# Performance work log

Measured on AMD Instinct MI355X. Metric: run time of the kernel, lower is better.

The kernel has to match this reference:

```python
import jax, jax.numpy as jnp
import numpy as np

HIDDEN = 1024
D_INNER = 2048
DT_RANK = 64
STATE = 16
KCONV = 4


def setup_inputs() -> dict:
    key = jax.random.key(0)
    ks = jax.random.split(key, 9)
    s = lambda k, shape, sc=0.02: jax.random.normal(k, shape, dtype=jnp.float32) * sc
    return {
        "x": jax.random.normal(ks[0], (2, 1024, HIDDEN), dtype=jnp.float32),
        "in_proj_w": s(ks[1], (2 * D_INNER, HIDDEN)),
        "conv_w": s(ks[2], (D_INNER, 1, KCONV), 0.2),
        "conv_b": s(ks[3], (D_INNER,), 0.1),
        "x_proj_w": s(ks[4], (DT_RANK + 2 * STATE, D_INNER)),
        "dt_proj_w": s(ks[5], (D_INNER, DT_RANK), 0.1),
        "dt_proj_b": s(ks[6], (D_INNER,), 0.1),
        "A_log": s(ks[7], (D_INNER, STATE), 0.5),
        "out_proj_w": s(ks[8], (HIDDEN, D_INNER)),
    }


def _selective_scan(u, delta, A, B, C):
    # u, delta: (b,l,d); A: (d,n); B, C: (b,l,n)
    deltaA = jnp.exp(delta[..., None] * A)               # (b,l,d,n)
    dBu = (delta * u)[..., None] * B[:, :, None, :]      # (b,l,d,n)
    # scan over time axis; carry h: (b,d,n)
    deltaA_t = jnp.moveaxis(deltaA, 1, 0)                # (l,b,d,n)
    dBu_t = jnp.moveaxis(dBu, 1, 0)                      # (l,b,d,n)
    C_t = jnp.moveaxis(C, 1, 0)                          # (l,b,n)

    def step(h, inp):
        dA_i, dBu_i, C_i = inp
        h = dA_i * h + dBu_i
        y = jnp.einsum('bdn,bn->bd', h, C_i)
        return h, y

    h0 = jnp.zeros(u.shape[:1] + u.shape[2:] + (A.shape[1],), dtype=u.dtype)
    _, ys = jax.lax.scan(step, h0, (deltaA_t, dBu_t, C_t))
    return jnp.moveaxis(ys, 0, 1)                        # (b,l,d)


def reference(x, in_proj_w, conv_w, conv_b, x_proj_w, dt_proj_w, dt_proj_b, A_log, out_proj_w):
    b, l, _ = x.shape
    xr = x @ in_proj_w.T                                 # (b,l,2*d_inner)
    xs, res = jnp.split(xr, 2, axis=-1)
    # causal depthwise conv1d: pad left k-1 (matches padding=k-1 then [:l])
    xc = jnp.moveaxis(xs, 1, 2)                          # (b,d,l)
    xc = jax.lax.conv_general_dilated(
        xc, conv_w, window_strides=(1,), padding=[(KCONV - 1, 0)],
        feature_group_count=D_INNER,
        dimension_numbers=('NCH', 'OIH', 'NCH'))
    xc = xc + conv_b[None, :, None]
    xs = jnp.moveaxis(xc, 2, 1)                          # (b,l,d)
    xs = jax.nn.silu(xs)
    x_dbl = xs @ x_proj_w.T                              # (b,l,dt_rank+2n)
    dt, B, C = jnp.split(x_dbl, [DT_RANK, DT_RANK + STATE], axis=-1)
    delta = jax.nn.softplus(dt @ dt_proj_w.T + dt_proj_b)
    A = -jnp.exp(A_log.astype(jnp.float32))
    y = _selective_scan(xs, delta, A, B, C)
    y = y * jax.nn.silu(res)
    return y @ out_proj_w.T
```

## Files before the change

### kernel.cpp

```cpp
#include <hip/hip_runtime.h>

typedef unsigned short u16;
typedef __bf16 bf16x8 __attribute__((ext_vector_type(8)));
typedef float f32x4 __attribute__((ext_vector_type(4)));

__device__ inline float bf2f(u16 u) {
    unsigned int x = ((unsigned int)u) << 16;
    return __builtin_bit_cast(float, x);
}
__device__ inline u16 f2bf(float f) {
    unsigned int x = __builtin_bit_cast(unsigned int, f);
    return (u16)((x + 0x7FFFu + ((x >> 16) & 1u)) >> 16);
}
__device__ inline float sigm(float v) { return 1.f / (1.f + __expf(-v)); }
__device__ inline float ex2(float x) {
    float r; asm("v_exp_f32 %0, %1" : "=v"(r) : "v"(x)); return r;
}

__device__ __forceinline__ void gload16(const void* g, void* l) {
    __builtin_amdgcn_global_load_lds(
        (const __attribute__((address_space(1))) void*)g,
        (__attribute__((address_space(3))) void*)l, 16, 0, 0);
}

__device__ inline uint4 pack8(const float* p) {
    const float4* q = (const float4*)p;
    float4 a = q[0], b = q[1];
    union { u16 h[8]; uint4 v; } u;
    u.h[0] = f2bf(a.x); u.h[1] = f2bf(a.y); u.h[2] = f2bf(a.z); u.h[3] = f2bf(a.w);
    u.h[4] = f2bf(b.x); u.h[5] = f2bf(b.y); u.h[6] = f2bf(b.z); u.h[7] = f2bf(b.w);
    return u.v;
}

__global__ __launch_bounds__(256)
void cvt_front(const float* __restrict__ x, const float* __restrict__ inw,
               const float* __restrict__ xpw, const float* __restrict__ convw,
               const float* __restrict__ dtw,
               u16* __restrict__ x_bf, u16* __restrict__ inw_bf,
               u16* __restrict__ xpw_bf, float* __restrict__ wt,
               u16* __restrict__ dtw_bf)
{
    int bk = blockIdx.x, tid = threadIdx.x;
    if (bk < 1024) {
        int i = bk * 256 + tid;
        ((uint4*)x_bf)[i] = pack8(x + (size_t)i * 8);
    } else if (bk < 3072) {
        int i = (bk - 1024) * 256 + tid;
        ((uint4*)inw_bf)[i] = pack8(inw + (size_t)i * 8);
    } else if (bk < 3200) {
        int i = (bk - 3072) * 256 + tid;
        int row = (i * 8) >> 11;
        ((uint4*)xpw_bf)[i] = (row < 96) ? pack8(xpw + (size_t)row * 2048 + ((i * 8) & 2047))
                                         : make_uint4(0u, 0u, 0u, 0u);
    } else if (bk < 3264) {
        int i = (bk - 3200) * 256 + tid;
        ((uint4*)dtw_bf)[i] = pack8(dtw + (size_t)i * 8);
    } else {
        int i = (bk - 3264) * 256 + tid;
        wt[(i & 3) * 2048 + (i >> 2)] = convw[i];
    }
}

__global__ __launch_bounds__(256)
void cvt_bf16(const float* __restrict__ in, u16* __restrict__ out)
{
    int i = blockIdx.x * 256 + threadIdx.x;
    ((uint4*)out)[i] = pack8(in + (size_t)i * 8);
}

template<int EPI, bool OUTF32>
__global__ __launch_bounds__(256, 4)
void gemm_w(const u16* __restrict__ A, int lda,
            const u16* __restrict__ B, int ldb,
            void* __restrict__ Cout, int ldc,
            int N, int ksplit, size_t zElems,
            const float* __restrict__ bias)
{
    __shared__ u16 sA[64][64];
    __shared__ u16 sB[128][64];

    const int tid  = threadIdx.x;
    const int lane = tid & 63;
    const int wave = tid >> 6;

    int nxy = gridDim.x * gridDim.y;
    int id  = blockIdx.y * gridDim.x + blockIdx.x;
    int bx, by;
    if ((nxy & 7) == 0) {
        int cpx = nxy >> 3;
        int swz = (id & 7) * cpx + (id >> 3);
        bx = swz % gridDim.x;
        by = swz / gridDim.x;
    } else { bx = blockIdx.x; by = blockIdx.y; }

    const int wm = (wave >> 1) * 32;
    const int wn = (wave & 1) * 64;
    const int m0 = by * 64;
    const int n0 = bx * 128;
    const int lm = lane & 15;
    const int g  = lane >> 4;
    const int k0 = blockIdx.z * ksplit;

    const int rr = lane >> 3;
    const int sl = lane & 7;
    const int xsl = sl ^ rr;
    const u16* gA = A + (size_t)(m0 + wave * 8 + rr) * lda + k0 + xsl * 8;
    const u16* gB = B + (size_t)(n0 + wave * 8 + rr) * ldb + k0 + xsl * 8;
    const int ldsRow = (wave * 8) * 128;

    f32x4 acc[2][4] = {};

    for (int kb = 0; kb < ksplit; kb += 64) {
        #pragma unroll
        for (int c = 0; c < 2; ++c)
            gload16(gA + (size_t)c * 32 * lda + kb, (char*)sA + c * 4096 + ldsRow);
        #pragma unroll
        for (int c = 0; c < 4; ++c)
            gload16(gB + (size_t)c * 32 * ldb + kb, (char*)sB + c * 4096 + ldsRow);
        __syncthreads();

        bf16x8 af[2][2], bfr[2][4];
        #pragma unroll
        for (int h = 0; h < 2; ++h) {
            int chunk = (((h << 2) | g) ^ (lm & 7)) << 4;
            #pragma unroll
            for (int i = 0; i < 2; ++i)
                af[h][i]  = *(const bf16x8*)((const char*)sA + (wm + i * 16 + lm) * 128 + chunk);
            #pragma unroll
            for (int j = 0; j < 4; ++j)
                bfr[h][j] = *(const bf16x8*)((const char*)sB + (wn + j * 16 + lm) * 128 + chunk);
        }
        #pragma unroll
        for (int h = 0; h < 2; ++h)
            #pragma unroll
            for (int i = 0; i < 2; ++i)
                #pragma unroll
                for (int j = 0; j < 4; ++j)
                    acc[i][j] = __builtin_amdgcn_mfma_f32_16x16x32_bf16(af[h][i], bfr[h][j], acc[i][j], 0, 0, 0);
        __syncthreads();
    }

    #pragma unroll
    for (int i = 0; i < 2; ++i) {
        int crow = m0 + wm + i * 16 + ((lane >> 4) << 2);
        #pragma unroll
        for (int j = 0; j < 4; ++j) {
            int ccol = n0 + wn + j * 16 + lm;
            if (ccol < N) {
                #pragma unroll
                for (int r = 0; r < 4; ++r) {
                    float v = acc[i][j][r];
                    if (EPI == 1) { v += bias[ccol]; v = (v > 20.f) ? v : log1pf(__expf(v)); }
                    if (EPI == 2 && ccol >= 2048) v *= sigm(v);
                    size_t off = (size_t)blockIdx.z * zElems + (size_t)(crow + r) * ldc + ccol;
                    if (OUTF32) ((float*)Cout)[off] = v;
                    else        ((u16*)Cout)[off]   = f2bf(v);
                }
            }
        }
    }
}

template<int EPI, bool OUTF32>
__global__ __launch_bounds__(256, 4)
void gemm_s(const u16* __restrict__ A, int lda,
            const u16* __restrict__ B, int ldb,
            void* __restrict__ Cout, int ldc,
            int N, int ksplit, size_t zElems,
            const float* __restrict__ bias)
{
    __shared__ u16 sA[64][64];
    __shared__ u16 sB[64][64];

    const int tid  = threadIdx.x;
    const int lane = tid & 63;
    const int wave = tid >> 6;

    int nxy = gridDim.x * gridDim.y;
    int id  = blockIdx.y * gridDim.x + blockIdx.x;
    int bx, by;
    if ((nxy & 7) == 0) {
        int cpx = nxy >> 3;
        int swz = (id & 7) * cpx + (id >> 3);
        bx = swz % gridDim.x;
        by = swz / gridDim.x;
    } else { bx = blockIdx.x; by = blockIdx.y; }

    const int wm = (wave >> 1) * 32;
    const int wn = (wave & 1) * 32;
    const int m0 = by * 64;
    const int n0 = bx * 64;
    const int lm = lane & 15;
    const int g  = lane >> 4;
    const int k0 = blockIdx.z * ksplit;

    const int rr = lane >> 3;
    const int sl = lane & 7;
    const int xsl = sl ^ rr;
    const u16* gA = A + (size_t)(m0 + wave * 8 + rr) * lda + k0 + xsl * 8;
    const u16* gB = B + (size_t)(n0 + wave * 8 + rr) * ldb + k0 + xsl * 8;
    const int ldsRow = (wave * 8) * 128;

    f32x4 acc[2][2] = {};

    for (int kb = 0; kb < ksplit; kb += 64) {
        #pragma unroll
        for (int c = 0; c < 2; ++c) {
            gload16(gA + (size_t)c * 32 * lda + kb, (char*)sA + c * 4096 + ldsRow);
            gload16(gB + (size_t)c * 32 * ldb + kb, (char*)sB + c * 4096 + ldsRow);
        }
        __syncthreads();

        bf16x8 af[2][2], bfr[2][2];
        #pragma unroll
        for (int h = 0; h < 2; ++h) {
            #pragma unroll
            for (int i = 0; i < 2; ++i) {
                int ra = wm + i * 16 + lm;
                int rb = wn + i * 16 + lm;
                int chunk = (((h << 2) | g) ^ (lm & 7)) << 4;
                af[h][i]  = *(const bf16x8*)((const char*)sA + ra * 128 + chunk);
                bfr[h][i] = *(const bf16x8*)((const char*)sB + rb * 128 + chunk);
            }
        }
        #pragma unroll
        for (int h = 0; h < 2; ++h)
            #pragma unroll
            for (int i = 0; i < 2; ++i)
                #pragma unroll
                for (int j = 0; j < 2; ++j)
                    acc[i][j] = __builtin_amdgcn_mfma_f32_16x16x32_bf16(af[h][i], bfr[h][j], acc[i][j], 0, 0, 0);
        __syncthreads();
    }

    #pragma unroll
    for (int i = 0; i < 2; ++i) {
        int crow = m0 + wm + i * 16 + ((lane >> 4) << 2);
        #pragma unroll
        for (int j = 0; j < 2; ++j) {
            int ccol = n0 + wn + j * 16 + lm;
            if (ccol < N) {
                #pragma unroll
                for (int r = 0; r < 4; ++r) {
                    float v = acc[i][j][r];
                    if (EPI == 1) { v += bias[ccol]; v = (v > 20.f) ? v : log1pf(__expf(v)); }
                    size_t off = (size_t)blockIdx.z * zElems + (size_t)(crow + r) * ldc + ccol;
                    if (OUTF32) ((float*)Cout)[off] = v;
                    else        ((u16*)Cout)[off]   = f2bf(v);
                }
            }
        }
    }
}

__global__ __launch_bounds__(256)
void reduce96(const float* __restrict__ splits, u16* __restrict__ xdbl)
{
    int i = blockIdx.x * 256 + threadIdx.x;
    float acc = 0.f;
    #pragma unroll
    for (int z = 0; z < 8; ++z) acc += splits[(size_t)z * 196608 + i];
    xdbl[i] = f2bf(acc);
}

__global__ __launch_bounds__(256)
void reduce_out(const u16* __restrict__ parts, float* __restrict__ out)
{
    int i = blockIdx.x * 256 + threadIdx.x;
    float acc[8] = {};
    #pragma unroll
    for (int z = 0; z < 4; ++z) {
        uint4 v = ((const uint4*)(parts + (size_t)z * 2097152))[i];
        const u16* h = (const u16*)&v;
        #pragma unroll
        for (int e = 0; e < 8; ++e) acc[e] += bf2f(h[e]);
    }
    float4* o = (float4*)(out + (size_t)i * 8);
    o[0] = make_float4(acc[0], acc[1], acc[2], acc[3]);
    o[1] = make_float4(acc[4], acc[5], acc[6], acc[7]);
}

__global__ __launch_bounds__(256)
void conv_silu(const u16* __restrict__ xr, const float* __restrict__ wt,
               const float* __restrict__ bias, u16* __restrict__ xs)
{
    int gi = blockIdx.x * 256 + threadIdx.x;
    int d  = (gi & 255) * 8;
    int t  = (gi >> 8) & 1023;
    int b  = gi >> 18;
    const u16* base = xr + (size_t)b * 4194304 + d;
    float acc[8];
    {
        const float4* bp = (const float4*)(bias + d);
        float4 b0 = bp[0], b1 = bp[1];
        acc[0]=b0.x; acc[1]=b0.y; acc[2]=b0.z; acc[3]=b0.w;
        acc[4]=b1.x; acc[5]=b1.y; acc[6]=b1.z; acc[7]=b1.w;
    }
    #pragma unroll
    for (int j = 0; j < 4; ++j) {
        int ti = t - 3 + j;
        if (ti >= 0) {
            uint4 v = *(const uint4*)(base + (size_t)ti * 4096);
            const u16* h = (const u16*)&v;
            const float4* wp = (const float4*)(wt + j * 2048 + d);
            float4 w0 = wp[0], w1 = wp[1];
            float w8[8] = {w0.x, w0.y, w0.z, w0.w, w1.x, w1.y, w1.z, w1.w};
            #pragma unroll
            for (int e = 0; e < 8; ++e) acc[e] = fmaf(w8[e], bf2f(h[e]), acc[e]);
        }
    }
    union { u16 h[8]; uint4 v; } o;
    #pragma unroll
    for (int e = 0; e < 8; ++e) { float v = acc[e]; o.h[e] = f2bf(v * sigm(v)); }
    ((uint4*)xs)[gi] = o.v;
}

template<int PHC>
__global__ __launch_bounds__(256)
void scan_chunk(const u16* __restrict__ deltag, u16* __restrict__ xsg,
                const u16* __restrict__ xdbl, const float* __restrict__ A_log,
                const u16* __restrict__ xr, float* __restrict__ summ,
                float* __restrict__ ssum)
{
    const int tid = threadIdx.x;
    const int d0 = blockIdx.x * 256;
    const int c  = blockIdx.y;
    const int b  = blockIdx.z;
    const int d  = d0 + tid;
    const int tok0 = b * 1024 + c * 32;

    __shared__ u16 s_del[32][256];
    __shared__ u16 s_uu[32][256];
    __shared__ u16 s_bc[32][32];
    __shared__ u16 s_res[PHC ? 32 : 1][PHC ? 256 : 1];
    __shared__ u16 s_y[PHC ? 32 : 1][PHC ? 256 : 1];

    for (int i = tid; i < 1024; i += 256) {
        int tl = i >> 5, v = i & 31;
        size_t tok = (size_t)(tok0 + tl);
        *(uint4*)&s_del[tl][v * 8] = *(const uint4*)&deltag[tok * 4096 + d0 + v * 8];
        *(uint4*)&s_uu[tl][v * 8]  = *(const uint4*)&xsg[tok * 2048 + d0 + v * 8];
        if (PHC)
            *(uint4*)&s_res[tl][v * 8] = *(const uint4*)&xr[tok * 4096 + 2048 + d0 + v * 8];
    }
    for (int i = tid; i < 1024; i += 256) {
        int tl = i >> 5, j = i & 31;
        s_bc[tl][j] = xdbl[(size_t)(tok0 + tl) * 96 + 64 + j];
    }

    float Ar[16], h[16];
    {
        const float4* Ap = (const float4*)(A_log + (size_t)d * 16);
        #pragma unroll
        for (int q = 0; q < 4; ++q) {
            float4 a = Ap[q];
            Ar[q * 4 + 0] = -__expf(a.x) * 1.44269504f;
            Ar[q * 4 + 1] = -__expf(a.y) * 1.44269504f;
            Ar[q * 4 + 2] = -__expf(a.z) * 1.44269504f;
            Ar[q * 4 + 3] = -__expf(a.w) * 1.44269504f;
        }
    }
    if (PHC) {
        const float4* hp = (const float4*)&summ[((size_t)(b * 32 + c) * 2048 + d) * 16];
        #pragma unroll
        for (int q = 0; q < 4; ++q) {
            float4 v = hp[q];
            h[q * 4 + 0] = v.x; h[q * 4 + 1] = v.y; h[q * 4 + 2] = v.z; h[q * 4 + 3] = v.w;
        }
    } else {
        #pragma unroll
        for (int n = 0; n < 16; ++n) h[n] = 0.f;
    }
    __syncthreads();

    float S = 0.f;
    #pragma unroll 4
    for (int tl = 0; tl < 32; ++tl) {
        float dlt = bf2f(s_del[tl][tid]);
        float du = dlt * bf2f(s_uu[tl][tid]);
        if (!PHC) S += dlt;
        #pragma unroll
        for (int n = 0; n < 16; ++n)
            h[n] = fmaf(ex2(dlt * Ar[n]), h[n], du * bf2f(s_bc[tl][n]));
        if (PHC) {
            float y = 0.f;
            #pragma unroll
            for (int n = 0; n < 16; ++n)
                y = fmaf(h[n], bf2f(s_bc[tl][16 + n]), y);
            s_y[tl][tid] = f2bf(y * bf2f(s_res[tl][tid]));
        }
    }

    if (!PHC) {
        float4* bp = (float4*)&summ[((size_t)(b * 32 + c) * 2048 + d) * 16];
        #pragma unroll
        for (int q = 0; q < 4; ++q)
            bp[q] = make_float4(h[q * 4], h[q * 4 + 1], h[q * 4 + 2], h[q * 4 + 3]);
        ssum[(size_t)(b * 32 + c) * 2048 + d] = S;
    } else {
        __syncthreads();
        for (int i = tid; i < 1024; i += 256) {
            int tl = i >> 5, v = i & 31;
            *(uint4*)&xsg[(size_t)(tok0 + tl) * 2048 + d0 + v * 8] = *(uint4*)&s_y[tl][v * 8];
        }
    }
}

__global__ __launch_bounds__(256)
void scan_phaseB(float* __restrict__ summ, const float* __restrict__ ssum,
                 const float* __restrict__ A_log)
{
    int g = blockIdx.x * 256 + threadIdx.x;
    int n = g & 15;
    int d = (g >> 4) & 2047;
    int b = g >> 15;
    float An2 = -__expf(A_log[(size_t)d * 16 + n]) * 1.44269504f;
    size_t base = ((size_t)(b * 32) * 2048 + d) * 16 + n;
    float bc[32], Sc[32];
    #pragma unroll
    for (int c = 0; c < 32; ++c) bc[c] = summ[base + (size_t)c * 32768];
    #pragma unroll
    for (int c = 0; c < 32; ++c) Sc[c] = ssum[(size_t)(b * 32 + c) * 2048 + d];
    float h = 0.f;
    #pragma unroll
    for (int c = 0; c < 32; ++c) {
        float nb = bc[c];
        bc[c] = h;
        h = fmaf(ex2(An2 * Sc[c]), h, nb);
    }
    #pragma unroll
    for (int c = 0; c < 32; ++c) summ[base + (size_t)c * 32768] = bc[c];
}

__global__ void sentinel_kernel(float* out, float v) { out[0] = v; }

extern "C" void kernel_launch(void* const* d_in, const int* in_sizes, int n_in,
                              void* d_out, int out_size, void* d_ws, size_t ws_size,
                              hipStream_t stream)
{
    const float* x         = (const float*)d_in[0];
    const float* in_w      = (const float*)d_in[1];
    const float* conv_w    = (const float*)d_in[2];
    const float* conv_b    = (const float*)d_in[3];
    const float* xproj_w   = (const float*)d_in[4];
    const float* dtproj_w  = (const float*)d_in[5];
    const float* dtproj_b  = (const float*)d_in[6];
    const float* A_log     = (const float*)d_in[7];
    const float* outproj_w = (const float*)d_in[8];
    float* out = (float*)d_out;

    static const int EXP[9] = {2097152, 4194304, 8192, 2048, 196608, 131072, 2048, 32768, 2097152};
    int bad = -1;
    if (n_in != 9) bad = 9;
    else { for (int i = 0; i < 9; ++i) if (in_sizes[i] != EXP[i]) { bad = i; break; } }
    if (bad < 0 && out_size != 2097152) bad = 10;
    if (bad < 0 && ws_size < 34734080u) bad = 11;
    if (bad >= 0) {
        sentinel_kernel<<<1, 1, 0, stream>>>(out, 131072.f * (1.f + (float)bad / 16.f));
        return;
    }

    char* ws = (char*)d_ws;
    u16*   xr      = (u16*)(ws);
    u16*   xs      = (u16*)(ws + 16777216);
    u16*   xdbl    = (u16*)(ws + 25165824);
    char*  R       = ws + 25559040;
    u16*   x_bf    = xs;
    u16*   inw_bf  = (u16*)(R);
    u16*   xpw_bf  = (u16*)(R + 8388608);
    float* wt      = (float*)(R + 8912896);
    u16*   dtw_bf  = (u16*)out;
    float* splits  = (float*)(R);
    float* summ    = (float*)(R);
    float* ssum    = (float*)(R + 8388608);
    u16*   opw_bf  = (u16*)(R);
    u16*   oparts  = xr;

    cvt_front<<<3296, 256, 0, stream>>>(x, in_w, xproj_w, conv_w, dtproj_w,
                                        x_bf, inw_bf, xpw_bf, wt, dtw_bf);
    gemm_w<2, false><<<dim3(32, 32, 1), 256, 0, stream>>>(
        x_bf, 1024, inw_bf, 1024, xr, 4096, 4096, 1024, 0, nullptr);
    conv_silu<<<2048, 256, 0, stream>>>(xr, wt, conv_b, xs);
    gemm_s<0, true><<<dim3(2, 32, 8), 256, 0, stream>>>(
        xs, 2048, xpw_bf, 2048, splits, 96, 96, 256, 196608, nullptr);
    reduce96<<<768, 256, 0, stream>>>(splits, xdbl);
    gemm_s<1, false><<<dim3(32, 32, 1), 256, 0, stream>>>(
        xdbl, 96, dtw_bf, 64, xr, 4096, 2048, 64, 0, dtproj_b);
    scan_chunk<0><<<dim3(8, 32, 2), 256, 0, stream>>>(xr, xs, xdbl, A_log, xr, summ, ssum);
    scan_phaseB<<<256, 256, 0, stream>>>(summ, ssum, A_log);
    scan_chunk<1><<<dim3(8, 32, 2), 256, 0, stream>>>(xr, xs, xdbl, A_log, xr, summ, ssum);
    cvt_bf16<<<1024, 256, 0, stream>>>(outproj_w, opw_bf);
    gemm_w<0, false><<<dim3(8, 32, 4), 256, 0, stream>>>(
        xs, 2048, opw_bf, 2048, oparts, 1024, 1024, 512, 2097152, nullptr);
    reduce_out<<<1024, 256, 0, stream>>>(oparts, out);
}
```

Baseline: 228.4 us.

## Fold out_proj weight conversion into front converter, vectorise reductions, reuse conv loads

The out_proj weight conversion moves into the single front conversion kernel and is staged in the output buffer, which removes a separate launch. reduce96 now handles 8 elements per thread with float4 loads. conv_silu computes 4 timesteps per thread so overlapping input rows are reused. The final GEMM switches to the gemm_s variant with a 2-way k-split instead of 4-way, which halves the partial sums reduce_out must add. Staging the bf16 weight in the output buffer assumes nothing overwrites it before the final GEMM reads it, and reduce_out writes out after that GEMM has consumed it.

```diff
diff --git a/kernel.cpp b/kernel.cpp
--- a/kernel.cpp
+++ b/kernel.cpp
@@ -35,10 +35,10 @@
 __global__ __launch_bounds__(256)
 void cvt_front(const float* __restrict__ x, const float* __restrict__ inw,
                const float* __restrict__ xpw, const float* __restrict__ convw,
-               const float* __restrict__ dtw,
+               const float* __restrict__ dtw, const float* __restrict__ opw,
                u16* __restrict__ x_bf, u16* __restrict__ inw_bf,
                u16* __restrict__ xpw_bf, float* __restrict__ wt,
-               u16* __restrict__ dtw_bf)
+               u16* __restrict__ dtw_bf, u16* __restrict__ opw_bf)
 {
     int bk = blockIdx.x, tid = threadIdx.x;
     if (bk < 1024) {
@@ -55,17 +55,13 @@
     } else if (bk < 3264) {
         int i = (bk - 3200) * 256 + tid;
         ((uint4*)dtw_bf)[i] = pack8(dtw + (size_t)i * 8);
+    } else if (bk < 4288) {
+        int i = (bk - 3264) * 256 + tid;
+        ((uint4*)opw_bf)[i] = pack8(opw + (size_t)i * 8);
     } else {
-        int i = (bk - 3264) * 256 + tid;
+        int i = (bk - 4288) * 256 + tid;
         wt[(i & 3) * 2048 + (i >> 2)] = convw[i];
     }
-}
-
-__global__ __launch_bounds__(256)
-void cvt_bf16(const float* __restrict__ in, u16* __restrict__ out)
-{
-    int i = blockIdx.x * 256 + threadIdx.x;
-    ((uint4*)out)[i] = pack8(in + (size_t)i * 8);
 }
 
 template<int EPI, bool OUTF32>
@@ -257,10 +253,18 @@
 void reduce96(const float* __restrict__ splits, u16* __restrict__ xdbl)
 {
     int i = blockIdx.x * 256 + threadIdx.x;
-    float acc = 0.f;
-    #pragma unroll
-    for (int z = 0; z < 8; ++z) acc += splits[(size_t)z * 196608 + i];
-    xdbl[i] = f2bf(acc);
+    float acc[8] = {};
+    #pragma unroll
+    for (int z = 0; z < 8; ++z) {
+        const float4* p = (const float4*)(splits + (size_t)z * 196608 + (size_t)i * 8);
+        float4 a = p[0], b = p[1];
+        acc[0] += a.x; acc[1] += a.y; acc[2] += a.z; acc[3] += a.w;
+        acc[4] += b.x; acc[5] += b.y; acc[6] += b.z; acc[7] += b.w;
+    }
+    union { u16 h[8]; uint4 v; } o;
+    #pragma unroll
+    for (int e = 0; e < 8; ++e) o.h[e] = f2bf(acc[e]);
+    ((uint4*)xdbl)[i] = o.v;
 }
 
 __global__ __launch_bounds__(256)
@@ -269,7 +273,7 @@
     int i = blockIdx.x * 256 + threadIdx.x;
     float acc[8] = {};
     #pragma unroll
-    for (int z = 0; z < 4; ++z) {
+    for (int z = 0; z < 2; ++z) {
         uint4 v = ((const uint4*)(parts + (size_t)z * 2097152))[i];
         const u16* h = (const u16*)&v;
         #pragma unroll
@@ -286,33 +290,49 @@
 {
     int gi = blockIdx.x * 256 + threadIdx.x;
     int d  = (gi & 255) * 8;
-    int t  = (gi >> 8) & 1023;
-    int b  = gi >> 18;
+    int t0 = ((gi >> 8) & 255) * 4;
+    int b  = gi >> 16;
     const u16* base = xr + (size_t)b * 4194304 + d;
-    float acc[8];
+
+    float bi[8], w8[4][8];
     {
         const float4* bp = (const float4*)(bias + d);
         float4 b0 = bp[0], b1 = bp[1];
-        acc[0]=b0.x; acc[1]=b0.y; acc[2]=b0.z; acc[3]=b0.w;
-        acc[4]=b1.x; acc[5]=b1.y; acc[6]=b1.z; acc[7]=b1.w;
-    }
-    #pragma unroll
-    for (int j = 0; j < 4; ++j) {
-        int ti = t - 3 + j;
-        if (ti >= 0) {
-            uint4 v = *(const uint4*)(base + (size_t)ti * 4096);
-            const u16* h = (const u16*)&v;
+        bi[0]=b0.x; bi[1]=b0.y; bi[2]=b0.z; bi[3]=b0.w;
+        bi[4]=b1.x; bi[5]=b1.y; bi[6]=b1.z; bi[7]=b1.w;
+        #pragma unroll
+        for (int j = 0; j < 4; ++j) {
             const float4* wp = (const float4*)(wt + j * 2048 + d);
             float4 w0 = wp[0], w1 = wp[1];
-            float w8[8] = {w0.x, w0.y, w0.z, w0.w, w1.x, w1.y, w1.z, w1.w};
-            #pragma unroll
-            for (int e = 0; e < 8; ++e) acc[e] = fmaf(w8[e], bf2f(h[e]), acc[e]);
-        }
-    }
-    union { u16 h[8]; uint4 v; } o;
-    #pragma unroll
-    for (int e = 0; e < 8; ++e) { float v = acc[e]; o.h[e] = f2bf(v * sigm(v)); }
-    ((uint4*)xs)[gi] = o.v;
+            w8[j][0]=w0.x; w8[j][1]=w0.y; w8[j][2]=w0.z; w8[j][3]=w0.w;
+            w8[j][4]=w1.x; w8[j][5]=w1.y; w8[j][6]=w1.z; w8[j][7]=w1.w;
+        }
+    }
+
+    uint4 v[7];
+    #pragma unroll
+    for (int r = 0; r < 7; ++r) {
+        int ti = t0 - 3 + r;
+        v[r] = (ti >= 0) ? *(const uint4*)(base + (size_t)ti * 4096)
+                         : make_uint4(0u, 0u, 0u, 0u);
+    }
+
+    #pragma unroll
+    for (int tt = 0; tt < 4; ++tt) {
+        float acc[8];
+        #pragma unroll
+        for (int e = 0; e < 8; ++e) acc[e] = bi[e];
+        #pragma unroll
+        for (int j = 0; j < 4; ++j) {
+            const u16* h = (const u16*)&v[tt + j];
+            #pragma unroll
+            for (int e = 0; e < 8; ++e) acc[e] = fmaf(w8[j][e], bf2f(h[e]), acc[e]);
+        }
+        union { u16 h[8]; uint4 u; } o;
+        #pragma unroll
+        for (int e = 0; e < 8; ++e) { float x = acc[e]; o.h[e] = f2bf(x * sigm(x)); }
+        *(uint4*)(xs + (size_t)b * 2097152 + (size_t)(t0 + tt) * 2048 + d) = o.u;
+    }
 }
 
 template<int PHC>
@@ -470,27 +490,26 @@
     u16*   xpw_bf  = (u16*)(R + 8388608);
     float* wt      = (float*)(R + 8912896);
     u16*   dtw_bf  = (u16*)out;
+    u16*   opw_bf  = (u16*)((char*)out + 262144);
     float* splits  = (float*)(R);
     float* summ    = (float*)(R);
     float* ssum    = (float*)(R + 8388608);
-    u16*   opw_bf  = (u16*)(R);
     u16*   oparts  = xr;
 
-    cvt_front<<<3296, 256, 0, stream>>>(x, in_w, xproj_w, conv_w, dtproj_w,
-                                        x_bf, inw_bf, xpw_bf, wt, dtw_bf);
+    cvt_front<<<4320, 256, 0, stream>>>(x, in_w, xproj_w, conv_w, dtproj_w, outproj_w,
+                                        x_bf, inw_bf, xpw_bf, wt, dtw_bf, opw_bf);
     gemm_w<2, false><<<dim3(32, 32, 1), 256, 0, stream>>>(
         x_bf, 1024, inw_bf, 1024, xr, 4096, 4096, 1024, 0, nullptr);
-    conv_silu<<<2048, 256, 0, stream>>>(xr, wt, conv_b, xs);
+    conv_silu<<<512, 256, 0, stream>>>(xr, wt, conv_b, xs);
     gemm_s<0, true><<<dim3(2, 32, 8), 256, 0, stream>>>(
         xs, 2048, xpw_bf, 2048, splits, 96, 96, 256, 196608, nullptr);
-    reduce96<<<768, 256, 0, stream>>>(splits, xdbl);
+    reduce96<<<96, 256, 0, stream>>>(splits, xdbl);
     gemm_s<1, false><<<dim3(32, 32, 1), 256, 0, stream>>>(
         xdbl, 96, dtw_bf, 64, xr, 4096, 2048, 64, 0, dtproj_b);
     scan_chunk<0><<<dim3(8, 32, 2), 256, 0, stream>>>(xr, xs, xdbl, A_log, xr, summ, ssum);
     scan_phaseB<<<256, 256, 0, stream>>>(summ, ssum, A_log);
     scan_chunk<1><<<dim3(8, 32, 2), 256, 0, stream>>>(xr, xs, xdbl, A_log, xr, summ, ssum);
-    cvt_bf16<<<1024, 256, 0, stream>>>(outproj_w, opw_bf);
-    gemm_w<0, false><<<dim3(8, 32, 4), 256, 0, stream>>>(
-        xs, 2048, opw_bf, 2048, oparts, 1024, 1024, 512, 2097152, nullptr);
+    gemm_s<0, false><<<dim3(16, 32, 2), 256, 0, stream>>>(
+        xs, 2048, opw_bf, 2048, oparts, 1024, 1024, 1024, 2097152, nullptr);
     reduce_out<<<1024, 256, 0, stream>>>(oparts, out);
 }
```

Measured after the change: 220.9 us. 1.03x faster.
